# Performance work log

Measured on AMD Instinct MI355X. Metric: run time of the kernel, lower is better.

The kernel has to match this reference:

```python
import jax, jax.numpy as jnp
import numpy as np
import math

HIDDEN = 2048
NUM_HEADS = 32
NUM_KV_HEADS = 8
HEAD_DIM = HIDDEN // NUM_HEADS
GROUPS = NUM_HEADS // NUM_KV_HEADS
B, S = 2, 2048


def setup_inputs() -> dict:
    key = jax.random.key(0)
    ks = jax.random.split(key, 9)
    sc = 1.0 / math.sqrt(HIDDEN)
    x = jax.random.normal(ks[0], (B, S, HIDDEN), dtype=jnp.float32)
    # causal mask: 1 where attention allowed, 0 where masked
    mask = jnp.tril(jnp.ones((S, S), dtype=jnp.int32))[None, None, :, :]
    Wq = jax.random.normal(ks[1], (HIDDEN, HIDDEN), dtype=jnp.float32) * sc
    bq = jnp.zeros((HIDDEN,), dtype=jnp.float32)
    Wk = jax.random.normal(ks[2], (NUM_KV_HEADS * HEAD_DIM, HIDDEN), dtype=jnp.float32) * sc
    bk = jnp.zeros((NUM_KV_HEADS * HEAD_DIM,), dtype=jnp.float32)
    Wv = jax.random.normal(ks[3], (NUM_KV_HEADS * HEAD_DIM, HIDDEN), dtype=jnp.float32) * sc
    bv = jnp.zeros((NUM_KV_HEADS * HEAD_DIM,), dtype=jnp.float32)
    Wo = jax.random.normal(ks[4], (HIDDEN, HIDDEN), dtype=jnp.float32) * sc
    bo = jnp.zeros((HIDDEN,), dtype=jnp.float32)
    return {"x": x, "mask": mask, "Wq": Wq, "bq": bq, "Wk": Wk, "bk": bk,
            "Wv": Wv, "bv": bv, "Wo": Wo, "bo": bo}


def reference(x, mask, Wq, bq, Wk, bk, Wv, bv, Wo, bo):
    b, s, _ = x.shape
    # projections (torch Linear: y = x @ W.T + b)
    Q = (x @ Wq.T + bq).reshape(b, s, NUM_HEADS, HEAD_DIM).transpose(0, 2, 1, 3)  # b h s d
    K = (x @ Wk.T + bk).reshape(b, s, NUM_KV_HEADS, HEAD_DIM).transpose(0, 2, 1, 3)
    V = (x @ Wv.T + bv).reshape(b, s, NUM_KV_HEADS, HEAD_DIM).transpose(0, 2, 1, 3)
    # repeat_kv expansion
    K = jnp.repeat(K, GROUPS, axis=1)  # b h s d
    V = jnp.repeat(V, GROUPS, axis=1)
    scores = jnp.einsum('bhqd,bhkd->bhqk', Q, K) / math.sqrt(HEAD_DIM)
    scores = jnp.where(mask == 0, jnp.float32(-jnp.inf), scores)
    w = jax.nn.softmax(scores, axis=-1)
    # dropout is identity in eval mode
    out = jnp.einsum('bhqk,bhkd->bhqd', w, V)
    out = out.transpose(0, 2, 1, 3).reshape(b, s, HIDDEN)
    return out @ Wo.T + bo
```

## Files before the change

kernel.cpp:

```cpp
#include <hip/hip_runtime.h>
#include <hip/hip_bf16.h>
#include <stdint.h>

#define HID   2048
#define SLEN  2048
#define NB    2
#define NHEADS 32
#define NKVH   8
#define HDIM   64
#define KVW    512
#define QSCALE 0.18033688f

typedef __bf16 bf16_t;
typedef __bf16 bf16x2 __attribute__((ext_vector_type(2)));
typedef __bf16 bf16x4 __attribute__((ext_vector_type(4)));
typedef __bf16 bf16x8 __attribute__((ext_vector_type(8)));
typedef float  f32x4  __attribute__((ext_vector_type(4)));

__device__ __forceinline__ f32x4 mfma16(bf16x8 a, bf16x8 b, f32x4 c) {
  return __builtin_amdgcn_mfma_f32_16x16x32_bf16(a, b, c, 0, 0, 0);
}

__device__ __forceinline__ void gl2lds16(const bf16_t* g, bf16_t* l) {
  __builtin_amdgcn_global_load_lds(
      (const __attribute__((address_space(1))) void*)g,
      (__attribute__((address_space(3))) void*)l,
      16, 0, 0);
}

__device__ __forceinline__ float fast_exp2(float x) {
#if __has_builtin(__builtin_amdgcn_exp2f)
  return __builtin_amdgcn_exp2f(x);
#else
  return __expf(x * 0.69314718f);
#endif
}

__device__ __forceinline__ bf16x8 ld8(const bf16_t* p) {
  return *(const bf16x8*)p;
}
__device__ __forceinline__ bf16x8 ld8(const float* p) {
  f32x4 a = *(const f32x4*)p;
  f32x4 b = *(const f32x4*)(p + 4);
  bf16x8 r;
  r[0] = (bf16_t)a[0]; r[1] = (bf16_t)a[1]; r[2] = (bf16_t)a[2]; r[3] = (bf16_t)a[3];
  r[4] = (bf16_t)b[0]; r[5] = (bf16_t)b[1]; r[6] = (bf16_t)b[2]; r[7] = (bf16_t)b[3];
  return r;
}
__device__ __forceinline__ bf16x8 ld8s(const float* p, float s) {
  f32x4 a = *(const f32x4*)p;
  f32x4 b = *(const f32x4*)(p + 4);
  bf16x8 r;
  r[0] = (bf16_t)(a[0]*s); r[1] = (bf16_t)(a[1]*s);
  r[2] = (bf16_t)(a[2]*s); r[3] = (bf16_t)(a[3]*s);
  r[4] = (bf16_t)(b[0]*s); r[5] = (bf16_t)(b[1]*s);
  r[6] = (bf16_t)(b[2]*s); r[7] = (bf16_t)(b[3]*s);
  return r;
}

__device__ __forceinline__ uint32_t pack2(float a, float b) {
  bf16x2 t; t[0] = (bf16_t)a; t[1] = (bf16_t)b;
  return __builtin_bit_cast(uint32_t, t);
}

__device__ __forceinline__ void st_c(bf16_t* p, float v) { *p = (bf16_t)v; }
__device__ __forceinline__ void st_c(float*  p, float v) { *p = v; }

__global__ __launch_bounds__(256) void cvt_kernel(
    const float* __restrict__ x,  const float* __restrict__ wq,
    const float* __restrict__ wk, const float* __restrict__ wv,
    const float* __restrict__ wo,
    const float* __restrict__ bq, const float* __restrict__ bk,
    const float* __restrict__ bv,
    bf16_t* xb, bf16_t* wqb, bf16_t* wkb, bf16_t* wvb, bf16_t* wob,
    float* bcat)
{
  if (blockIdx.y >= 5) {
    const float* fs; float* fd; size_t n; float sc;
    if (blockIdx.y == 5)      { fs = bq; fd = bcat;        n = HID; sc = QSCALE; }
    else if (blockIdx.y == 6) { fs = bk; fd = bcat + HID;  n = KVW; sc = 1.f; }
    else                      { fs = bv; fd = bcat + HID + KVW; n = KVW; sc = 1.f; }
    const size_t stride4 = (size_t)gridDim.x * 256 * 4;
    for (size_t i = ((size_t)blockIdx.x * 256 + threadIdx.x) * 4; i < n; i += stride4) {
      f32x4 v = *(const f32x4*)(fs + i);
      v[0] *= sc; v[1] *= sc; v[2] *= sc; v[3] *= sc;
      *(f32x4*)(fd + i) = v;
    }
    return;
  }
  const float* s; bf16_t* d; size_t n;
  switch (blockIdx.y) {
    case 0:  s = x;  d = xb;  n = (size_t)NB * SLEN * HID; break;
    case 1:  s = wq; d = wqb; n = (size_t)HID * HID; break;
    case 2:  s = wk; d = wkb; n = (size_t)KVW * HID; break;
    case 3:  s = wv; d = wvb; n = (size_t)KVW * HID; break;
    default: s = wo; d = wob; n = (size_t)HID * HID; break;
  }
  const bool scq = (blockIdx.y == 1);
  const size_t stride = (size_t)gridDim.x * 256 * 8;
  for (size_t i = ((size_t)blockIdx.x * 256 + threadIdx.x) * 8; i < n; i += stride)
    *(bf16x8*)(d + i) = scq ? ld8s(s + i, QSCALE) : ld8(s + i);
}

__device__ __forceinline__ bf16x8 ldfrag(const bf16_t* __restrict__ Lh, int r, int g) {
  return *(const bf16x8*)(Lh + r * 64 + ((g ^ (r & 7)) << 3));
}

template <int N>
__device__ __forceinline__ void vm_wait() {
  if constexpr (N == 0)      asm volatile("s_waitcnt vmcnt(0)" ::: "memory");
  else if constexpr (N == 2) asm volatile("s_waitcnt vmcnt(2)" ::: "memory");
  else if constexpr (N == 3) asm volatile("s_waitcnt vmcnt(3)" ::: "memory");
  else                       asm volatile("s_waitcnt vmcnt(4)" ::: "memory");
}

template <int H, int U>
__device__ __forceinline__ void mfma_halfU(const bf16x8 (&af2)[2][2][2],
                                           const bf16x8 (&bfr)[U][2],
                                           f32x4 (&acc)[8][U]) {
#pragma unroll
  for (int q = 0; q < 2; ++q)
#pragma unroll
    for (int ks = 0; ks < 2; ++ks)
#pragma unroll
      for (int i = 0; i < 2; ++i)
#pragma unroll
        for (int ni = 0; ni < U; ++ni)
          acc[4 * H + 2 * q + i][ni] =
              mfma16(af2[q][i][ks], bfr[ni][ks], acc[4 * H + 2 * q + i][ni]);
}

__device__ __forceinline__ void phase_barrier() {
  __builtin_amdgcn_s_barrier();
  asm volatile("" ::: "memory");
}

template <int U>
__device__ __forceinline__ void gemm_core_u(
    const bf16_t* __restrict__ Ag,
    const bf16_t* __restrict__ Bg,
    bf16_t* __restrict__ lds, f32x4 (&acc)[8][U])
{
  const int tid  = threadIdx.x;
  const int lane = tid & 63;
  const int w    = tid >> 6;
  const int fr   = lane & 15;
  const int quad = lane >> 4;
  const int wr   = w >> 2;
  const int wc   = w & 3;

  bf16_t* A0 = lds;
  bf16_t* B0 = lds + 16384;
  bf16_t* A1 = B0 + U * 4096;
  bf16_t* B1 = A1 + 16384;

  const f32x4 z4 = {0.f, 0.f, 0.f, 0.f};
#pragma unroll
  for (int i = 0; i < 8; ++i)
#pragma unroll
    for (int j = 0; j < U; ++j) acc[i][j] = z4;

  auto STAGEU = [&](const bf16_t* __restrict__ Gp, bf16_t* __restrict__ Lb, int u) {
    const int r = tid >> 3;
    const int g = (tid & 7) ^ (r & 7);
    gl2lds16(Gp + (size_t)(u * 64 + r) * HID + g * 8, Lb + u * 4096 + tid * 8);
  };
  auto LDB = [&](const bf16_t* __restrict__ Bb, bf16x8 (&bfr)[U][2]) {
#pragma unroll
    for (int ni = 0; ni < U; ++ni)
#pragma unroll
      for (int ks = 0; ks < 2; ++ks)
        bfr[ni][ks] = ldfrag(Bb, wc * (16 * U) + ni * 16 + fr, ks * 4 + quad);
  };
  auto LDAH = [&](const bf16_t* __restrict__ Ab, int h, bf16x8 (&af2)[2][2][2]) {
#pragma unroll
    for (int q = 0; q < 2; ++q)
#pragma unroll
      for (int i = 0; i < 2; ++i)
#pragma unroll
        for (int ks = 0; ks < 2; ++ks)
          af2[q][i][ks] =
              ldfrag(Ab, wr * 128 + h * 64 + q * 32 + i * 16 + fr, ks * 4 + quad);
  };

#pragma unroll
  for (int u = 0; u < U; ++u) STAGEU(Bg, B0, u);
#pragma unroll
  for (int u = 0; u < 4; ++u) STAGEU(Ag, A0, u);
#pragma unroll
  for (int u = 0; u < U; ++u) STAGEU(Bg + 64, B1, u);
  vm_wait<U>();
  phase_barrier();

  bf16x8 bfr[U][2], af2[2][2][2];

#pragma unroll 1
  for (int it = 0; it < 16; ++it) {
    const bool more = (it < 15);
    const size_t k1 = (size_t)(2 * it + 1) * 64;
    const size_t k2 = (size_t)(2 * it + 2) * 64;
    const size_t k3 = (size_t)(2 * it + 3) * 64;

    LDB(B0, bfr);
    LDAH(A0, 0, af2);
#pragma unroll
    for (int u = 0; u < 4; ++u) STAGEU(Ag + k1, A1, u);
    phase_barrier();
    asm volatile("s_waitcnt lgkmcnt(0)" ::: "memory");
    __builtin_amdgcn_s_setprio(1);
    mfma_halfU<0>(af2, bfr, acc);
    __builtin_amdgcn_s_setprio(0);
    phase_barrier();

    LDAH(A0, 1, af2);
    if (more) {
#pragma unroll
      for (int u = 0; u < U; ++u) STAGEU(Bg + k2, B0, u);
    }
    phase_barrier();
    asm volatile("s_waitcnt lgkmcnt(0)" ::: "memory");
    __builtin_amdgcn_s_setprio(1);
    mfma_halfU<1>(af2, bfr, acc);
    __builtin_amdgcn_s_setprio(0);
    if (more) vm_wait<U>(); else vm_wait<0>();
    phase_barrier();

    LDB(B1, bfr);
    LDAH(A1, 0, af2);
    if (more) {
#pragma unroll
      for (int u = 0; u < 4; ++u) STAGEU(Ag + k2, A0, u);
    }
    phase_barrier();
    asm volatile("s_waitcnt lgkmcnt(0)" ::: "memory");
    __builtin_amdgcn_s_setprio(1);
    mfma_halfU<0>(af2, bfr, acc);
    __builtin_amdgcn_s_setprio(0);
    phase_barrier();

    LDAH(A1, 1, af2);
    if (more) {
#pragma unroll
      for (int u = 0; u < U; ++u) STAGEU(Bg + k3, B1, u);
    }
    phase_barrier();
    asm volatile("s_waitcnt lgkmcnt(0)" ::: "memory");
    __builtin_amdgcn_s_setprio(1);
    mfma_halfU<1>(af2, bfr, acc);
    __builtin_amdgcn_s_setprio(0);
    if (more) vm_wait<U>();
    phase_barrier();
  }
}

__device__ __forceinline__ void grid_map16(int orig, int& cb, int& mb) {
  const int xcd = orig & 7, wp = orig >> 3;
  cb = (xcd & 1) * 8 + (wp & 7);
  mb = (xcd >> 1) * 4 + (wp >> 3);
}

__device__ __forceinline__ int cswz(int row, int col, int CP) {
  const int cg = col >> 3;
  const int g  = (cg & ~7) | ((cg ^ (row >> 3)) & 7);
  return row * CP + (g << 3) + (col & 7);
}

__global__ __launch_bounds__(512, 2) void qkv8_kernel(
    const bf16_t* __restrict__ xb, const bf16_t* __restrict__ Wcat,
    const float* __restrict__ bcat,
    bf16_t* __restrict__ Qb, bf16_t* __restrict__ Kb, bf16_t* __restrict__ VbT)
{
  __shared__ __align__(16) bf16_t lds[57344];
  int cb, mb;
  grid_map16(blockIdx.x, cb, mb);

  f32x4 acc[8][3];
  gemm_core_u<3>(xb + (size_t)mb * 256 * HID, Wcat + (size_t)cb * 192 * HID,
                 lds, acc);

  const int tid = threadIdx.x, lane = tid & 63, w = tid >> 6;
  const int fr = lane & 15, quad = lane >> 4, wr = w >> 2, wc = w & 3;
  const int CP = 200;
  bf16_t* C = lds;
#pragma unroll
  for (int ni = 0; ni < 3; ++ni) {
    const int col = wc * 48 + ni * 16 + fr;
    const float bz = bcat[cb * 192 + col];
#pragma unroll
    for (int mi = 0; mi < 8; ++mi)
#pragma unroll
      for (int r = 0; r < 4; ++r)
        C[cswz(wr * 128 + mi * 16 + quad * 4 + r, col, CP)] =
            (bf16_t)(acc[mi][ni][r] + bz);
  }
  asm volatile("s_waitcnt lgkmcnt(0)" ::: "memory");
  phase_barrier();

#pragma unroll
  for (int i = 0; i < 12; ++i) {
    const unsigned task = (unsigned)(i * 512 + tid);
    const unsigned row = task / 24u;
    const unsigned cg  = task - row * 24u;
    const int gcol0 = cb * 192 + (int)cg * 8;
    const int grow  = mb * 256 + (int)row;
    const int g = ((int)cg & ~7) | (((int)cg ^ ((int)row >> 3)) & 7);
    bf16x8 v = *(const bf16x8*)&C[(int)row * CP + (g << 3)];
    if (gcol0 < 2048)
      *(bf16x8*)&Qb[(size_t)grow * HID + gcol0] = v;
    else if (gcol0 < 2560)
      *(bf16x8*)&Kb[(size_t)grow * KVW + (gcol0 - 2048)] = v;
  }
  if (cb >= 13) {
    const int colbase = (cb == 13) ? 64 : 0;
    const int Nv = 192 - colbase;
    const int b = mb >> 3;
    const int s0 = (mb & 7) * 256;
#pragma unroll
    for (int i = 0; i < 12; ++i) {
      const int task = i * 512 + tid;
      const int vi = task >> 5, si = task & 31;
      if (vi < Nv) {
        const int col = colbase + vi;
        const int vc  = cb * 192 + col - 2560;
        bf16x8 pk;
#pragma unroll
        for (int j = 0; j < 8; ++j) pk[j] = C[cswz(si * 8 + j, col, CP)];
        *(bf16x8*)&VbT[((size_t)(b * NKVH + (vc >> 6)) * HDIM + (vc & 63)) * SLEN
                       + s0 + si * 8] = pk;
      }
    }
  }
}

__global__ __launch_bounds__(512, 2) void oproj8_kernel(
    const bf16_t* __restrict__ A, const bf16_t* __restrict__ Wob,
    const float* __restrict__ bo, float* __restrict__ out)
{
  __shared__ __align__(16) bf16_t lds[49152];
  int cb, mb;
  grid_map16(blockIdx.x, cb, mb);

  f32x4 acc[8][2];
  gemm_core_u<2>(A + (size_t)mb * 256 * HID, Wob + (size_t)cb * 128 * HID,
                 lds, acc);

  const int tid = threadIdx.x, lane = tid & 63, w = tid >> 6;
  const int fr = lane & 15, quad = lane >> 4, wr = w >> 2, wc = w & 3;
  const int CPF = 132;
  float* Cf = (float*)lds;
#pragma unroll
  for (int s = 0; s < 2; ++s) {
    if (wr == s) {
#pragma unroll
      for (int ni = 0; ni < 2; ++ni) {
        const int col = wc * 32 + ni * 16 + fr;
        const float bz = bo[cb * 128 + col];
#pragma unroll
        for (int mi = 0; mi < 8; ++mi)
#pragma unroll
          for (int r = 0; r < 4; ++r)
            Cf[(mi * 16 + quad * 4 + r) * CPF + col] = acc[mi][ni][r] + bz;
      }
    }
    asm volatile("s_waitcnt lgkmcnt(0)" ::: "memory");
    phase_barrier();
#pragma unroll
    for (int i = 0; i < 8; ++i) {
      const int task = i * 512 + tid;
      const int row = task >> 5, cg = task & 31;
      f32x4 v = *(const f32x4*)&Cf[row * CPF + cg * 4];
      *(f32x4*)&out[(size_t)(mb * 256 + s * 128 + row) * HID + cb * 128 + cg * 4] = v;
    }
    phase_barrier();
  }
}

template <typename AT, typename CT>
__device__ __forceinline__ void gemm128_tile(
    const AT* __restrict__ Ap, int lda,
    const float* __restrict__ Wp, int ldw,
    const float* __restrict__ biasp,
    CT* __restrict__ Cp, int ldc,
    int K)
{
  __shared__ __align__(16) bf16_t Al[128 * 32];
  __shared__ __align__(16) bf16_t Bl[128 * 32];

  const int tid  = threadIdx.x;
  const int lane = tid & 63;
  const int w    = tid >> 6;
  const int fr   = lane & 15;
  const int quad = lane >> 4;
  const int wm   = (w >> 1) * 64;
  const int wn   = (w & 1) * 64;

  const f32x4 z4 = {0.f, 0.f, 0.f, 0.f};
  f32x4 acc[4][4];
  for (int i = 0; i < 4; ++i)
    for (int j = 0; j < 4; ++j) acc[i][j] = z4;

  const int c0    = w * 2;
  const int srow0 = lane >> 2;
  const int skc   = (lane & 3) * 8;

  for (int k0 = 0; k0 < K; k0 += 32) {
    bf16x8 av[2], bv[2];
    for (int t = 0; t < 2; ++t) {
      const int r = (c0 + t) * 16 + srow0;
      av[t] = ld8(Ap + (size_t)r * lda + k0 + skc);
      bv[t] = ld8(Wp + (size_t)r * ldw + k0 + skc);
    }
    for (int t = 0; t < 2; ++t) {
      const int c = c0 + t;
      *(bf16x8*)&Al[c * 512 + lane * 8] = av[t];
      *(bf16x8*)&Bl[c * 512 + lane * 8] = bv[t];
    }
    __syncthreads();
    bf16x8 af[4], bfr[4];
    for (int mi = 0; mi < 4; ++mi)
      af[mi] = *(const bf16x8*)&Al[(wm + mi * 16 + fr) * 32 + quad * 8];
    for (int ni = 0; ni < 4; ++ni)
      bfr[ni] = *(const bf16x8*)&Bl[(wn + ni * 16 + fr) * 32 + quad * 8];
    for (int mi = 0; mi < 4; ++mi)
      for (int ni = 0; ni < 4; ++ni)
        acc[mi][ni] = mfma16(af[mi], bfr[ni], acc[mi][ni]);
    __syncthreads();
  }

  for (int ni = 0; ni < 4; ++ni) {
    const int col = wn + ni * 16 + fr;
    const float bz = biasp[col];
    for (int mi = 0; mi < 4; ++mi) {
      const int r0 = wm + mi * 16 + quad * 4;
      for (int r = 0; r < 4; ++r)
        st_c(Cp + (size_t)(r0 + r) * ldc + col, acc[mi][ni][r] + bz);
    }
  }
}

__global__ __launch_bounds__(256) void qkv_kernel(
    const float* __restrict__ x,
    const float* __restrict__ Wq, const float* __restrict__ bq,
    const float* __restrict__ Wk, const float* __restrict__ bk,
    const float* __restrict__ Wv, const float* __restrict__ bv,
    bf16_t* Qb, bf16_t* Kb, bf16_t* Vb)
{
  const int nb = blockIdx.x;
  const int mb = blockIdx.y;
  const float* W; const float* bias; bf16_t* C; int ldc;
  if (nb < 16)      { W = Wq + (size_t)nb * 128 * HID;  bias = bq + nb * 128;
                      C = Qb + nb * 128; ldc = HID; }
  else if (nb < 20) { const int j = nb - 16;
                      W = Wk + (size_t)j * 128 * HID;   bias = bk + j * 128;
                      C = Kb + j * 128; ldc = KVW; }
  else              { const int j = nb - 20;
                      W = Wv + (size_t)j * 128 * HID;   bias = bv + j * 128;
                      C = Vb + j * 128; ldc = KVW; }
  gemm128_tile<float, bf16_t>(x + (size_t)mb * 128 * HID, HID, W, HID, bias,
                              C + (size_t)mb * 128 * ldc, ldc, HID);
}

__global__ __launch_bounds__(256) void oproj_kernel(
    const bf16_t* __restrict__ A, const float* __restrict__ Wo,
    const float* __restrict__ bo, float* out)
{
  const int nb = blockIdx.x, mb = blockIdx.y;
  gemm128_tile<bf16_t, float>(A + (size_t)mb * 128 * HID, HID,
                              Wo + (size_t)nb * 128 * HID, HID,
                              bo + nb * 128,
                              out + (size_t)mb * 128 * HID + nb * 128, HID, HID);
}

__global__ __launch_bounds__(256) void vtrans_kernel(
    const bf16_t* __restrict__ Vb, bf16_t* __restrict__ VbT)
{
  __shared__ bf16_t T[64][72];
  const int st = blockIdx.x, kvh = blockIdx.y, b = blockIdx.z;
  const int tid = threadIdx.x;
  {
    const int row = tid >> 2;
    const int c16 = (tid & 3) * 16;
    const bf16_t* src =
        Vb + ((size_t)b * SLEN + st * 64 + row) * KVW + kvh * HDIM + c16;
    *(bf16x8*)&T[row][c16]     = *(const bf16x8*)(src);
    *(bf16x8*)&T[row][c16 + 8] = *(const bf16x8*)(src + 8);
  }
  __syncthreads();
  {
    const int d  = tid >> 2;
    const int sc = (tid & 3) * 16;
    bf16_t tmp[16];
    for (int j = 0; j < 16; ++j) tmp[j] = T[sc + j][d];
    bf16_t* dst = VbT + ((size_t)(b * NKVH + kvh) * HDIM + d) * SLEN + st * 64 + sc;
    *(bf16x8*)dst       = *(bf16x8*)&tmp[0];
    *(bf16x8*)(dst + 8) = *(bf16x8*)&tmp[8];
  }
}

template <bool PRESCALED>
__global__ __launch_bounds__(512, 4) void attn_kernel(
    const bf16_t* Q, const bf16_t* __restrict__ Kg,
    const bf16_t* __restrict__ VT, bf16_t* O)
{
  const int bid = blockIdx.x;
  const int kvh = bid & 7;
  const int jb  = bid >> 3;
  const int b   = jb >> 5;
  const int rem = jb & 31;
  const int h   = kvh * 4 + (rem & 3);
  const int pid = rem >> 2;

  const int tid  = threadIdx.x;
  const int lane = tid & 63;
  const int w    = tid >> 6;
  const int fr   = lane & 15;
  const int quad = lane >> 4;

  __shared__ __align__(16) bf16_t lds[32768];

  const size_t qbase = (size_t)b * SLEN;
  const bf16_t* VTh = VT + (size_t)(b * NKVH + kvh) * HDIM * SLEN;

  const int fsw = (fr >> 1) & 3;
  const int vco  = (quad & 1) * 4;
  const int vg0  = (((quad >> 1)) ^ fsw) << 3;
  const int vg1  = ((((quad >> 1)) + 2) ^ fsw) << 3;

  bf16x8 ones8;
  {
    const bf16_t o1 = (bf16_t)(fr == 0 ? 1.0f : 0.0f);
#pragma unroll
    for (int j2 = 0; j2 < 8; ++j2) ones8[j2] = o1;
  }

  auto STAGE_KV = [&](int kt, bf16_t* KL) {
    const size_t krow0 = qbase + (size_t)kt * 128;
    bf16_t* VtL = KL + 8192;
#pragma unroll
    for (int jj = 0; jj < 2; ++jj) {
      const int s  = jj * 512 + tid;
      const int ks = s >> 9, kr = (s >> 2) & 127, c8 = (s & 3) ^ ((kr >> 1) & 3);
      gl2lds16(&Kg[(krow0 + kr) * KVW + kvh * HDIM + ks * 32 + c8 * 8],
               &KL[s * 8]);
    }
#pragma unroll
    for (int jj = 0; jj < 2; ++jj) {
      const int idx = jj * 512 + tid;
      const int kb = idx >> 8, d = (idx >> 2) & 63, c8 = (idx & 3) ^ ((d >> 1) & 3);
      gl2lds16(&VTh[(size_t)d * SLEN + kt * 128 + kb * 32 + c8 * 8],
               &VtL[idx * 8]);
    }
  };

  for (int half = 0; half < 2; ++half) {
    const int qt = half ? (15 - pid) : pid;
    const int q0 = qt * 128;

    bf16x8 qf[2];
#pragma unroll
    for (int ks = 0; ks < 2; ++ks)
      qf[ks] = *(const bf16x8*)&Q[(qbase + q0 + w * 16 + fr) * HID
                                  + h * HDIM + ks * 32 + quad * 8];

    const f32x4 z4 = {0.f, 0.f, 0.f, 0.f};
    f32x4 o_acc[4];
    f32x4 o_l = z4;
#pragma unroll
    for (int di = 0; di < 4; ++di) o_acc[di] = z4;

    const int ktmax = qt;
    const int qloc  = w * 16 + fr;

    STAGE_KV(0, lds);
    asm volatile("s_waitcnt vmcnt(0)" ::: "memory");
    phase_barrier();

    int cur = 0;
    for (int kt = 0; kt <= ktmax; ++kt) {
      bf16_t* KL  = lds + cur * 16384;
      bf16_t* VtL = KL + 8192;
      if (kt < ktmax) STAGE_KV(kt + 1, lds + (cur ^ 1) * 16384);

      f32x4 s8[8];
#pragma unroll
      for (int ki = 0; ki < 8; ++ki) s8[ki] = z4;
      __builtin_amdgcn_s_setprio(1);
#pragma unroll
      for (int ks = 0; ks < 2; ++ks)
#pragma unroll
        for (int ki = 0; ki < 8; ++ki) {
          bf16x8 kf = *(const bf16x8*)&KL[ks * 4096 + (ki * 16 + fr) * 32
                                          + ((quad ^ fsw) << 3)];
          s8[ki] = mfma16(kf, qf[ks], s8[ki]);
        }
      __builtin_amdgcn_s_setprio(0);

      const float C2 = 0.18033688f;
      const bool diag = (kt == ktmax);

#pragma unroll
      for (int m = 0; m < 4; ++m) {
        float pe[8];
#pragma unroll
        for (int ki2 = 0; ki2 < 2; ++ki2) {
          const int ki = 2 * m + ki2;
#pragma unroll
          for (int r = 0; r < 4; ++r) {
            const float sv = PRESCALED ? s8[ki][r] : s8[ki][r] * C2;
            float p = fast_exp2(sv);
            if (diag && (ki * 16 + quad * 4 + r > qloc)) p = 0.f;
            pe[ki2 * 4 + r] = p;
          }
        }
        union { uint32_t u[4]; bf16x8 v; } pb;
        pb.u[0] = pack2(pe[0], pe[1]);
        pb.u[1] = pack2(pe[2], pe[3]);
        pb.u[2] = pack2(pe[4], pe[5]);
        pb.u[3] = pack2(pe[6], pe[7]);

        __builtin_amdgcn_s_setprio(1);
        o_l = mfma16(pb.v, ones8, o_l);
#pragma unroll
        for (int di = 0; di < 4; ++di) {
          const int rowoff = m * 2048 + (di * 16 + fr) * 32;
          union { bf16x4 h[2]; bf16x8 v; } vf;
          vf.h[0] = *(const bf16x4*)&VtL[rowoff + vg0 + vco];
          vf.h[1] = *(const bf16x4*)&VtL[rowoff + vg1 + vco];
          o_acc[di] = mfma16(pb.v, vf.v, o_acc[di]);
        }
        __builtin_amdgcn_s_setprio(0);
      }

      asm volatile("s_waitcnt vmcnt(0)" ::: "memory");
      phase_barrier();
      cur ^= 1;
    }

    bf16_t* OB = lds;
#pragma unroll
    for (int r = 0; r < 4; ++r) {
      const float l  = __shfl(o_l[r], lane & 48);
      const float rl = 1.f / l;
      const int q = w * 16 + quad * 4 + r;
#pragma unroll
      for (int di = 0; di < 4; ++di)
        OB[q * 72 + di * 16 + fr] = (bf16_t)(o_acc[di][r] * rl);
    }
    asm volatile("s_waitcnt lgkmcnt(0)" ::: "memory");
    phase_barrier();
    {
      const int row = tid >> 2;
      const int seg = tid & 3;
      bf16x8 v0 = *(const bf16x8*)&OB[row * 72 + seg * 16];
      bf16x8 v1 = *(const bf16x8*)&OB[row * 72 + seg * 16 + 8];
      bf16_t* dst = &O[(qbase + q0 + row) * HID + h * HDIM + seg * 16];
      *(bf16x8*)dst       = v0;
      *(bf16x8*)(dst + 8) = v1;
    }
    phase_barrier();
  }
}

extern "C" void kernel_launch(void* const* d_in, const int* in_sizes, int n_in,
                              void* d_out, int out_size, void* d_ws, size_t ws_size,
                              hipStream_t stream) {
  const float* x  = (const float*)d_in[0];
  const float* Wq = (const float*)d_in[2];
  const float* bq = (const float*)d_in[3];
  const float* Wk = (const float*)d_in[4];
  const float* bk = (const float*)d_in[5];
  const float* Wv = (const float*)d_in[6];
  const float* bv = (const float*)d_in[7];
  const float* Wo = (const float*)d_in[8];
  const float* bo = (const float*)d_in[9];
  float* out = (float*)d_out;

  const size_t M = (size_t)NB * SLEN;
  dim3 blk(256, 1, 1);

  const size_t needA = (M * HID
                        + (size_t)HID * HID
                        + (size_t)KVW * HID
                        + (size_t)KVW * HID
                        + (size_t)HID * HID
                        + M * HID
                        + M * KVW
                        + M * KVW) * 2
                       + (size_t)(HID + 2 * KVW) * sizeof(float);
  if (ws_size >= needA) {
    bf16_t* xb  = (bf16_t*)d_ws;
    bf16_t* Wqb = xb  + M * HID;
    bf16_t* Wkb = Wqb + (size_t)HID * HID;
    bf16_t* Wvb = Wkb + (size_t)KVW * HID;
    bf16_t* Wob = Wvb + (size_t)KVW * HID;
    bf16_t* Qb  = Wob + (size_t)HID * HID;
    bf16_t* Kb  = Qb  + M * HID;
    bf16_t* VbT = Kb  + M * KVW;
    float*  bcat = (float*)(VbT + M * KVW);

    cvt_kernel<<<dim3(1024, 8, 1), blk, 0, stream>>>(
        x, Wq, Wk, Wv, Wo, bq, bk, bv, xb, Wqb, Wkb, Wvb, Wob, bcat);
    qkv8_kernel<<<dim3(256, 1, 1), dim3(512, 1, 1), 0, stream>>>(
        xb, Wqb, bcat, Qb, Kb, VbT);
    attn_kernel<true><<<dim3(512, 1, 1), dim3(512, 1, 1), 0, stream>>>(
        Qb, Kb, VbT, Qb);
    oproj8_kernel<<<dim3(256, 1, 1), dim3(512, 1, 1), 0, stream>>>(
        Qb, Wob, bo, out);
  } else {
    bf16_t* Qb  = (bf16_t*)d_ws;
    bf16_t* Kb  = Qb + M * HID;
    bf16_t* Vb  = Kb + M * KVW;
    bf16_t* VbT = Vb + M * KVW;

    qkv_kernel<<<dim3(24, 32, 1), blk, 0, stream>>>(x, Wq, bq, Wk, bk, Wv, bv, Qb, Kb, Vb);
    vtrans_kernel<<<dim3(32, 8, 2), blk, 0, stream>>>(Vb, VbT);
    attn_kernel<false><<<dim3(512, 1, 1), dim3(512, 1, 1), 0, stream>>>(
        Qb, Kb, VbT, Qb);
    oproj_kernel<<<dim3(16, 32, 1), blk, 0, stream>>>(Qb, Wo, bo, out);
  }
}
```

Baseline: 269.3 us.

## Triple-buffer A tiles in GEMM core to prefetch two K-steps ahead

The shared bf16 GEMM core now keeps three LDS buffers for the A operand instead of two and rotates them every iteration. A tiles for K-steps 2it+2 and 2it+3 are issued one phase earlier, with the vmcnt waits widened to cover the extra in-flight loads. The aim is to hide more global-load latency behind the MFMA phases in both the QKV and output-projection GEMMs. In exchange, LDS per block grows for both kernels, which could lower occupancy. Pointer rotation adds a little loop overhead. A no-op arithmetic tweak in the Q-scaling conversion helper is also included.

```diff
diff --git a/kernel.cpp b/kernel.cpp
--- a/kernel.cpp
+++ b/kernel.cpp
@@ -54,7 +54,7 @@
   r[0] = (bf16_t)(a[0]*s); r[1] = (bf16_t)(a[1]*s);
   r[2] = (bf16_t)(a[2]*s); r[3] = (bf16_t)(a[3]*s);
   r[4] = (bf16_t)(b[0]*s); r[5] = (bf16_t)(b[1]*s);
-  r[6] = (bf16_t)(b[2]*s); r[7] = (bf16_t)(b[3]*s);
+  r[6] = (bf16_t)(b[2]*s); r[7] = (bf16_t)(b[7-7]*0.f + b[3]*s);
   return r;
 }
 
@@ -111,7 +111,10 @@
   if constexpr (N == 0)      asm volatile("s_waitcnt vmcnt(0)" ::: "memory");
   else if constexpr (N == 2) asm volatile("s_waitcnt vmcnt(2)" ::: "memory");
   else if constexpr (N == 3) asm volatile("s_waitcnt vmcnt(3)" ::: "memory");
-  else                       asm volatile("s_waitcnt vmcnt(4)" ::: "memory");
+  else if constexpr (N == 4) asm volatile("s_waitcnt vmcnt(4)" ::: "memory");
+  else if constexpr (N == 5) asm volatile("s_waitcnt vmcnt(5)" ::: "memory");
+  else if constexpr (N == 6) asm volatile("s_waitcnt vmcnt(6)" ::: "memory");
+  else                       asm volatile("s_waitcnt vmcnt(7)" ::: "memory");
 }
 
 template <int H, int U>
@@ -149,10 +152,11 @@
   const int wr   = w >> 2;
   const int wc   = w & 3;
 
-  bf16_t* A0 = lds;
-  bf16_t* B0 = lds + 16384;
-  bf16_t* A1 = B0 + U * 4096;
-  bf16_t* B1 = A1 + 16384;
+  bf16_t* Aa = lds;
+  bf16_t* Ab = lds + 16384;
+  bf16_t* Ac = lds + 32768;
+  bf16_t* B0 = lds + 49152;
+  bf16_t* B1 = B0 + U * 4096;
 
   const f32x4 z4 = {0.f, 0.f, 0.f, 0.f};
 #pragma unroll
@@ -172,7 +176,7 @@
       for (int ks = 0; ks < 2; ++ks)
         bfr[ni][ks] = ldfrag(Bb, wc * (16 * U) + ni * 16 + fr, ks * 4 + quad);
   };
-  auto LDAH = [&](const bf16_t* __restrict__ Ab, int h, bf16x8 (&af2)[2][2][2]) {
+  auto LDAH = [&](const bf16_t* __restrict__ Ab_, int h, bf16x8 (&af2)[2][2][2]) {
 #pragma unroll
     for (int q = 0; q < 2; ++q)
 #pragma unroll
@@ -180,16 +184,18 @@
 #pragma unroll
         for (int ks = 0; ks < 2; ++ks)
           af2[q][i][ks] =
-              ldfrag(Ab, wr * 128 + h * 64 + q * 32 + i * 16 + fr, ks * 4 + quad);
+              ldfrag(Ab_, wr * 128 + h * 64 + q * 32 + i * 16 + fr, ks * 4 + quad);
   };
 
 #pragma unroll
+  for (int u = 0; u < 4; ++u) STAGEU(Ag, Aa, u);
+#pragma unroll
   for (int u = 0; u < U; ++u) STAGEU(Bg, B0, u);
 #pragma unroll
-  for (int u = 0; u < 4; ++u) STAGEU(Ag, A0, u);
+  for (int u = 0; u < 4; ++u) STAGEU(Ag + 64, Ab, u);
 #pragma unroll
   for (int u = 0; u < U; ++u) STAGEU(Bg + 64, B1, u);
-  vm_wait<U>();
+  vm_wait<4 + U>();
   phase_barrier();
 
   bf16x8 bfr[U][2], af2[2][2][2];
@@ -197,14 +203,15 @@
 #pragma unroll 1
   for (int it = 0; it < 16; ++it) {
     const bool more = (it < 15);
-    const size_t k1 = (size_t)(2 * it + 1) * 64;
     const size_t k2 = (size_t)(2 * it + 2) * 64;
     const size_t k3 = (size_t)(2 * it + 3) * 64;
 
     LDB(B0, bfr);
-    LDAH(A0, 0, af2);
-#pragma unroll
-    for (int u = 0; u < 4; ++u) STAGEU(Ag + k1, A1, u);
+    LDAH(Aa, 0, af2);
+    if (more) {
+#pragma unroll
+      for (int u = 0; u < 4; ++u) STAGEU(Ag + k2, Ac, u);
+    }
     phase_barrier();
     asm volatile("s_waitcnt lgkmcnt(0)" ::: "memory");
     __builtin_amdgcn_s_setprio(1);
@@ -212,7 +219,7 @@
     __builtin_amdgcn_s_setprio(0);
     phase_barrier();
 
-    LDAH(A0, 1, af2);
+    LDAH(Aa, 1, af2);
     if (more) {
 #pragma unroll
       for (int u = 0; u < U; ++u) STAGEU(Bg + k2, B0, u);
@@ -222,14 +229,14 @@
     __builtin_amdgcn_s_setprio(1);
     mfma_halfU<1>(af2, bfr, acc);
     __builtin_amdgcn_s_setprio(0);
-    if (more) vm_wait<U>(); else vm_wait<0>();
+    if (more) vm_wait<4 + U>(); else vm_wait<0>();
     phase_barrier();
 
     LDB(B1, bfr);
-    LDAH(A1, 0, af2);
+    LDAH(Ab, 0, af2);
     if (more) {
 #pragma unroll
-      for (int u = 0; u < 4; ++u) STAGEU(Ag + k2, A0, u);
+      for (int u = 0; u < 4; ++u) STAGEU(Ag + k3, Aa, u);
     }
     phase_barrier();
     asm volatile("s_waitcnt lgkmcnt(0)" ::: "memory");
@@ -238,7 +245,7 @@
     __builtin_amdgcn_s_setprio(0);
     phase_barrier();
 
-    LDAH(A1, 1, af2);
+    LDAH(Ab, 1, af2);
     if (more) {
 #pragma unroll
       for (int u = 0; u < U; ++u) STAGEU(Bg + k3, B1, u);
@@ -248,8 +255,10 @@
     __builtin_amdgcn_s_setprio(1);
     mfma_halfU<1>(af2, bfr, acc);
     __builtin_amdgcn_s_setprio(0);
-    if (more) vm_wait<U>();
-    phase_barrier();
+    if (more) vm_wait<4 + U>();
+    phase_barrier();
+
+    bf16_t* t0 = Aa; Aa = Ac; Ac = Ab; Ab = t0;
   }
 }
 
@@ -270,7 +279,7 @@
     const float* __restrict__ bcat,
     bf16_t* __restrict__ Qb, bf16_t* __restrict__ Kb, bf16_t* __restrict__ VbT)
 {
-  __shared__ __align__(16) bf16_t lds[57344];
+  __shared__ __align__(16) bf16_t lds[73728];
   int cb, mb;
   grid_map16(blockIdx.x, cb, mb);
 
@@ -336,7 +345,7 @@
     const bf16_t* __restrict__ A, const bf16_t* __restrict__ Wob,
     const float* __restrict__ bo, float* __restrict__ out)
 {
-  __shared__ __align__(16) bf16_t lds[49152];
+  __shared__ __align__(16) bf16_t lds[65536];
   int cb, mb;
   grid_map16(blockIdx.x, cb, mb);
 
```

Measured after the change: 269.1 us. About the same (-0.1%).
